# Kernel optimization log

Hardware: AMD Instinct MI355X
Metric: run time of the kernel (lower is better)

Reference implementation:

```python
import jax, jax.numpy as jnp
import numpy as np

# irrep blocks for 0e+1o+2e: dims 1, 3, 5 (total D=9)
BLOCKS = [(0, 1), (1, 4), (4, 9)]

def block_linear(x, W):
    # x: [N, C, 9], W: [3, C, C] -- e3nn Linear mixes channels within each irrep block
    outs = [jnp.einsum('ncd,cq->nqd', x[..., s:e], W[l]) for l, (s, e) in enumerate(BLOCKS)]
    return jnp.concatenate(outs, axis=-1)

def setup_inputs() -> dict:
    key = jax.random.key(0)
    ks = jax.random.split(key, 14)
    N, E, C, D, B, H, Z = 16384, 262144, 32, 9, 8, 64, 4
    inp = {
        'node_feats': jax.random.normal(ks[0], (N, C, D), jnp.float32),
        'node_attrs': jax.random.uniform(ks[1], (N, Z), jnp.float32),
        'edge_feats': jax.random.normal(ks[2], (E, B), jnp.float32),
        'edge_sh': jax.random.normal(ks[3], (E, D), jnp.float32),
        'cutoff': jax.random.uniform(ks[4], (E, 1), jnp.float32),
        # learned params
        'W_up': jax.random.normal(ks[5], (3, C, C), jnp.float32) / np.float32(np.sqrt(C)),
        'W1': jax.random.normal(ks[6], (B, H), jnp.float32) / np.float32(np.sqrt(B)),
        'W2': jax.random.normal(ks[7], (H, H), jnp.float32) / np.float32(np.sqrt(H)),
        'W3': jax.random.normal(ks[8], (H, C), jnp.float32) / np.float32(np.sqrt(H)),
        'W_lin': jax.random.normal(ks[9], (3, C, C), jnp.float32) / np.float32(np.sqrt(C)),
        'W_sc': jax.random.normal(ks[10], (Z, 3, C, C), jnp.float32) / np.float32(np.sqrt(C)),
        # fixed Clebsch-Gordan-like coupling tensor (constant structure of the TP)
        'CG': jax.random.normal(ks[11], (D, D, D), jnp.float32) / np.float32(D),
        'edge_src': jax.random.randint(ks[12], (E,), 0, N, jnp.int32),
        'edge_dst': jax.random.randint(ks[13], (E,), 0, N, jnp.int32),
    }
    return inp

def reference(node_feats, node_attrs, edge_feats, edge_sh, cutoff,
              W_up, W1, W2, W3, W_lin, W_sc, CG, edge_src, edge_dst):
    N = node_feats.shape[0]
    avg_num_neighbors = 16.0
    # linear_up: per-irrep channel mixing
    x = block_linear(node_feats, W_up)
    # radial MLP -> per-edge tensor-product weights, gated by cutoff
    h = jax.nn.silu(edge_feats @ W1)
    h = jax.nn.silu(h @ W2)
    w = (h @ W3) * cutoff  # [E, C]
    # gather source node feats, weighted equivariant tensor product per edge
    xs = x[edge_src]  # [E, C, D]
    m_ij = jnp.einsum('eci,ej,ijk,ec->eck', xs, edge_sh, CG, w)  # [E, C, D]
    # scatter-sum aggregation into destination nodes
    m_i = jax.ops.segment_sum(m_ij, edge_dst, num_segments=N)  # [N, C, D]
    # output linear + neighbor normalization
    m_i = block_linear(m_i, W_lin) / avg_num_neighbors
    # element-dependent self-connection from current message
    W_node = jnp.einsum('nz,zlcq->nlcq', node_attrs, W_sc)  # [N, 3, C, C]
    scs = jnp.concatenate(
        [jnp.einsum('ncd,ncq->nqd', m_i[..., s:e], W_node[:, l]) for l, (s, e) in enumerate(BLOCKS)],
        axis=-1)
    return (m_i, scs)
```

## Files before the change

### kernel.cpp

```cpp
#include <hip/hip_runtime.h>
#include <cstdint>

#define CC 32
#define DD 9
#define CD 288
#define BB 8
#define HH 64
#define ZZ 4
#define NB 8

typedef __attribute__((ext_vector_type(8))) short bf16x8;
typedef __attribute__((ext_vector_type(4))) float f32x4;

__device__ __forceinline__ float silu_f(float v) {
  return v / (1.0f + __expf(-v));
}

__device__ __forceinline__ int blk_of(int d) { return d == 0 ? 0 : (d < 4 ? 1 : 2); }

__device__ __forceinline__ unsigned int f2bf(float f) {
  unsigned int u = __float_as_uint(f);
  return (u + 0x7fffu + ((u >> 16) & 1u)) >> 16;
}
__device__ __forceinline__ float bf_lo(unsigned int u) { return __uint_as_float(u << 16); }
__device__ __forceinline__ float bf_hi(unsigned int u) { return __uint_as_float(u & 0xffff0000u); }

__global__ __launch_bounds__(256) void k_zero(float* __restrict__ p, int n) {
  int i = blockIdx.x * 256 + threadIdx.x;
  if (i < n) p[i] = 0.0f;
}

__global__ __launch_bounds__(256) void k_hist(const int* __restrict__ edst,
                                              int* __restrict__ deg, int E) {
  int e = blockIdx.x * 256 + threadIdx.x;
  if (e < E) atomicAdd(&deg[edst[e]], 1);
}

__global__ __launch_bounds__(1024) void k_scan(const int* __restrict__ deg,
                                               int* __restrict__ offs,
                                               int* __restrict__ cursor, int N) {
  __shared__ int part[1024];
  int t = threadIdx.x;
  int chunk = (N + 1023) >> 10;
  int base = t * chunk;
  int lim = N - base; if (lim > chunk) lim = chunk; if (lim < 0) lim = 0;
  int s = 0;
  for (int i = 0; i < lim; ++i) s += deg[base + i];
  part[t] = s;
  __syncthreads();
  for (int off = 1; off < 1024; off <<= 1) {
    int v = part[t];
    int u = (t >= off) ? part[t - off] : 0;
    __syncthreads();
    part[t] = v + u;
    __syncthreads();
  }
  int run = (t == 0) ? 0 : part[t - 1];
  for (int i = 0; i < lim; ++i) {
    offs[base + i] = run;
    cursor[base + i] = run;
    run += deg[base + i];
  }
  if (t == 1023) offs[N] = run;
}

__global__ __launch_bounds__(256) void k_scatter(const int* __restrict__ edst,
                                                 const int* __restrict__ esrc,
                                                 int* __restrict__ cursor,
                                                 int* __restrict__ eidx,
                                                 int* __restrict__ srcs, int E) {
  int e = blockIdx.x * 256 + threadIdx.x;
  if (e < E) {
    int d = edst[e];
    int pos = atomicAdd(&cursor[d], 1);
    eidx[pos] = e;
    srcs[pos] = esrc[e];
  }
}

__global__ __launch_bounds__(256) void k_eshs(const int* __restrict__ eidx,
                                              const float* __restrict__ esh,
                                              unsigned int* __restrict__ esh_p, long total) {
  long i = (long)blockIdx.x * 256 + threadIdx.x;
  if (i < total) {
    long pos = i / 5;
    int jj = (int)(i - pos * 5);
    int e = eidx[pos];
    unsigned int lo = f2bf(esh[(size_t)e * 9 + 2 * jj]);
    unsigned int hi = (jj < 4) ? f2bf(esh[(size_t)e * 9 + 2 * jj + 1]) : 0u;
    esh_p[i] = lo | (hi << 16);
  }
}

__global__ __launch_bounds__(288) void k_linear_up(
    const float* __restrict__ nf, const float* __restrict__ Wup,
    unsigned int* __restrict__ x_p, int N) {
  __shared__ float snf[NB][DD * 36];
  __shared__ float sval[NB][DD][CC];
  int t = threadIdx.x;
  int g = t >> 5, q = t & 31;
  int tc = t / 9, td = t - tc * 9;
  int l0 = blk_of(g);
  float wcol[CC];
#pragma unroll
  for (int c = 0; c < CC; ++c) wcol[c] = Wup[l0 * 1024 + c * 32 + q];
  int n0 = blockIdx.x * NB;
#pragma unroll
  for (int nb = 0; nb < NB; ++nb) {
    if (n0 + nb < N) snf[nb][td * 36 + tc] = nf[(size_t)(n0 + nb) * CD + t];
  }
  __syncthreads();
#pragma unroll
  for (int nb = 0; nb < NB; ++nb) {
    if (n0 + nb >= N) break;
    const float4* rowp = (const float4*)(snf[nb] + g * 36);
    float a0 = 0.f, a1 = 0.f;
#pragma unroll
    for (int c4 = 0; c4 < 8; ++c4) {
      float4 b = rowp[c4];
      a0 += b.x * wcol[c4 * 4 + 0] + b.y * wcol[c4 * 4 + 1];
      a1 += b.z * wcol[c4 * 4 + 2] + b.w * wcol[c4 * 4 + 3];
    }
    sval[nb][g][q] = a0 + a1;
  }
  __syncthreads();
#pragma unroll
  for (int it = 0; it < 5; ++it) {
    int idx = it * 288 + t;
    if (idx < NB * 160) {
      int nb = idx / 160, r = idx - nb * 160;
      int p = r >> 5, c = r & 31;
      if (n0 + nb < N) {
        unsigned int lo = f2bf(sval[nb][2 * p][c]);
        unsigned int hi = (p < 4) ? f2bf(sval[nb][2 * p + 1][c]) : 0u;
        x_p[(size_t)(n0 + nb) * 160 + r] = lo | (hi << 16);
      }
    }
  }
}

__global__ __launch_bounds__(64) void k_mlp_mfma(
    const float* __restrict__ ef, const float* __restrict__ cut,
    const float* __restrict__ W1, const float* __restrict__ W2,
    const float* __restrict__ W3, const int* __restrict__ eidx,
    unsigned int* __restrict__ w_p, int E) {
  __shared__ ushort hbuf[4096];
  __shared__ ushort h2buf[4096];
  __shared__ float scut[64];
  int l = threadIdx.x;
  int h = l >> 4, li = l & 15;
  bf16x8 A2[4][2];
#pragma unroll
  for (int qm = 0; qm < 4; ++qm)
#pragma unroll
    for (int kb = 0; kb < 2; ++kb)
#pragma unroll
      for (int j = 0; j < 8; ++j)
        A2[qm][kb][j] = (short)f2bf(W2[(32 * kb + 8 * h + j) * HH + 16 * qm + li]);
  bf16x8 A3[2][2];
#pragma unroll
  for (int cm = 0; cm < 2; ++cm)
#pragma unroll
    for (int kb = 0; kb < 2; ++kb)
#pragma unroll
      for (int j = 0; j < 8; ++j)
        A3[cm][kb][j] = (short)f2bf(W3[(32 * kb + 8 * h + j) * CC + 16 * cm + li]);

  int ntile = E >> 6;
  for (int tile = blockIdx.x; tile < ntile; tile += gridDim.x) {
    int pos = tile * 64 + l;
    int eo = eidx[pos];
    const float4* efp = (const float4*)(ef + (size_t)eo * BB);
    float4 efa = efp[0];
    float4 efb = efp[1];
    scut[l] = cut[eo];
    float efv[BB] = {efa.x, efa.y, efa.z, efa.w, efb.x, efb.y, efb.z, efb.w};
#pragma unroll
    for (int g = 0; g < 8; ++g) {
      float hv[8];
#pragma unroll
      for (int jj = 0; jj < 8; ++jj) {
        int q = g * 8 + jj;
        float a = 0.f;
#pragma unroll
        for (int kin = 0; kin < BB; ++kin) a += efv[kin] * W1[kin * HH + q];
        hv[jj] = silu_f(a);
      }
      unsigned int d0 = f2bf(hv[0]) | (f2bf(hv[1]) << 16);
      unsigned int d1 = f2bf(hv[2]) | (f2bf(hv[3]) << 16);
      unsigned int d2 = f2bf(hv[4]) | (f2bf(hv[5]) << 16);
      unsigned int d3 = f2bf(hv[6]) | (f2bf(hv[7]) << 16);
      int F = ((l >> 4) * 2 + (g >> 2)) * 4 + (g & 3);
      *(uint4*)&hbuf[(F * 16 + li) * 8] = make_uint4(d0, d1, d2, d3);
    }
    f32x4 acc2[4][4];
#pragma unroll
    for (int qm = 0; qm < 4; ++qm)
#pragma unroll
      for (int nb = 0; nb < 4; ++nb) acc2[qm][nb] = (f32x4){0.f, 0.f, 0.f, 0.f};
#pragma unroll
    for (int nb = 0; nb < 4; ++nb)
#pragma unroll
      for (int kb = 0; kb < 2; ++kb) {
        int F = (nb * 2 + kb) * 4 + h;
        bf16x8 Bf = *(const bf16x8*)&hbuf[(F * 16 + li) * 8];
#pragma unroll
        for (int qm = 0; qm < 4; ++qm)
          acc2[qm][nb] = __builtin_amdgcn_mfma_f32_16x16x32_bf16(
              A2[qm][kb], Bf, acc2[qm][nb], 0, 0, 0);
      }
#pragma unroll
    for (int qm = 0; qm < 4; ++qm)
#pragma unroll
      for (int nb = 0; nb < 4; ++nb) {
        float v0 = silu_f(acc2[qm][nb][0]);
        float v1 = silu_f(acc2[qm][nb][1]);
        float v2 = silu_f(acc2[qm][nb][2]);
        float v3 = silu_f(acc2[qm][nb][3]);
        unsigned int lo = f2bf(v0) | (f2bf(v1) << 16);
        unsigned int hi = f2bf(v2) | (f2bf(v3) << 16);
        int G = (nb * 2 + (qm >> 1)) * 4 + ((2 * qm + (h >> 1)) & 3);
        *(uint2*)&h2buf[(G * 16 + li) * 8 + (h & 1) * 4] = make_uint2(lo, hi);
      }
    f32x4 acc3[2][4];
#pragma unroll
    for (int cm = 0; cm < 2; ++cm)
#pragma unroll
      for (int nb = 0; nb < 4; ++nb) acc3[cm][nb] = (f32x4){0.f, 0.f, 0.f, 0.f};
#pragma unroll
    for (int nb = 0; nb < 4; ++nb)
#pragma unroll
      for (int kb = 0; kb < 2; ++kb) {
        int G = (nb * 2 + kb) * 4 + h;
        bf16x8 Bf = *(const bf16x8*)&h2buf[(G * 16 + li) * 8];
#pragma unroll
        for (int cm = 0; cm < 2; ++cm)
          acc3[cm][nb] = __builtin_amdgcn_mfma_f32_16x16x32_bf16(
              A3[cm][kb], Bf, acc3[cm][nb], 0, 0, 0);
      }
#pragma unroll
    for (int nb = 0; nb < 4; ++nb) {
      float cv = scut[16 * nb + li];
#pragma unroll
      for (int cm = 0; cm < 2; ++cm) {
        unsigned int lo = f2bf(acc3[cm][nb][0] * cv) | (f2bf(acc3[cm][nb][1] * cv) << 16);
        unsigned int hi = f2bf(acc3[cm][nb][2] * cv) | (f2bf(acc3[cm][nb][3] * cv) << 16);
        *(uint2*)&w_p[(size_t)(tile * 64 + 16 * nb + li) * 16 + 8 * cm + 2 * h] =
            make_uint2(lo, hi);
      }
    }
  }
}

__global__ __launch_bounds__(256) void k_gather(
    const unsigned int* __restrict__ x_p, const unsigned int* __restrict__ w_p,
    const unsigned int* __restrict__ esh_p, const float* __restrict__ CG,
    const int* __restrict__ offs, const int* __restrict__ srcs,
    float* __restrict__ mpre, int N) {
  int wid = (blockIdx.x * 256 + threadIdx.x) >> 6;
  if (wid >= N) return;
  int lane = threadIdx.x & 63;
  int h = lane >> 5, c = lane & 31;
  int beg = offs[wid], end = offs[wid + 1];
  float P[81];
#pragma unroll
  for (int i = 0; i < 81; ++i) P[i] = 0.f;
  for (int p0 = beg; p0 < end; p0 += 2) {
    int p = p0 + h;
    bool ok = p < end;
    int pp = ok ? p : p0;
    int s = srcs[pp];
    unsigned int wu = w_p[(size_t)pp * 16 + (c >> 1)];
    float wc = ok ? ((c & 1) ? bf_hi(wu) : bf_lo(wu)) : 0.f;
    const unsigned int* shp = esh_p + (size_t)pp * 5;
    unsigned int s0 = shp[0], s1 = shp[1], s2 = shp[2], s3 = shp[3], s4 = shp[4];
    float sh[DD];
    sh[0] = bf_lo(s0); sh[1] = bf_hi(s0);
    sh[2] = bf_lo(s1); sh[3] = bf_hi(s1);
    sh[4] = bf_lo(s2); sh[5] = bf_hi(s2);
    sh[6] = bf_lo(s3); sh[7] = bf_hi(s3);
    sh[8] = bf_lo(s4);
    const unsigned int* xp = x_p + (size_t)s * 160 + c;
    unsigned int u0 = xp[0], u1 = xp[32], u2 = xp[64], u3 = xp[96], u4 = xp[128];
    float xs[DD];
    xs[0] = bf_lo(u0); xs[1] = bf_hi(u0);
    xs[2] = bf_lo(u1); xs[3] = bf_hi(u1);
    xs[4] = bf_lo(u2); xs[5] = bf_hi(u2);
    xs[6] = bf_lo(u3); xs[7] = bf_hi(u3);
    xs[8] = bf_lo(u4);
#pragma unroll
    for (int i = 0; i < DD; ++i) {
      float t = wc * xs[i];
#pragma unroll
      for (int j = 0; j < DD; ++j) P[i * DD + j] += t * sh[j];
    }
  }
  float m[DD];
#pragma unroll
  for (int k = 0; k < DD; ++k) m[k] = 0.f;
#pragma unroll
  for (int i = 0; i < DD; ++i) {
#pragma unroll
    for (int j = 0; j < DD; ++j) {
      float p = P[i * DD + j];
#pragma unroll
      for (int k = 0; k < DD; ++k) m[k] += p * CG[i * 81 + j * DD + k];
    }
  }
#pragma unroll
  for (int k = 0; k < DD; ++k) m[k] += __shfl_xor(m[k], 32);
  if (h == 0) {
    float* mp = mpre + (size_t)wid * CD + c;
#pragma unroll
    for (int k = 0; k < DD; ++k) mp[k * 32] = m[k];
  }
}

__global__ __launch_bounds__(288, 1) void k_out(
    const float* __restrict__ attrs, const float* __restrict__ Wlin,
    const float* __restrict__ Wsc,
    float* __restrict__ out1, float* __restrict__ out2, int N) {
  __shared__ float smp[NB][CD];
  __shared__ float smt[NB][CD];
  __shared__ float sres1[NB * CD];
  __shared__ float sres2[NB * CD];
  int t = threadIdx.x;
  int g = t >> 5, q = t & 31;
  int l0 = blk_of(g);
  float wl[CC];
#pragma unroll
  for (int c = 0; c < CC; ++c) wl[c] = Wlin[l0 * 1024 + c * 32 + q];
  float ws0[CC], ws1[CC], ws2[CC], ws3[CC];
#pragma unroll
  for (int c = 0; c < CC; ++c) {
    ws0[c] = Wsc[0 * 3072 + l0 * 1024 + c * 32 + q];
    ws1[c] = Wsc[1 * 3072 + l0 * 1024 + c * 32 + q];
    ws2[c] = Wsc[2 * 3072 + l0 * 1024 + c * 32 + q];
    ws3[c] = Wsc[3 * 3072 + l0 * 1024 + c * 32 + q];
  }
  int nbat = (N + NB - 1) / NB;
  int b = blockIdx.x;
  float r[NB];
  if (b < nbat) {
#pragma unroll
    for (int nb = 0; nb < NB; ++nb) r[nb] = out2[(size_t)(b * NB + nb) * CD + t];
  }
  for (; b < nbat; b += gridDim.x) {
    int n0 = b * NB;
    __syncthreads();
#pragma unroll
    for (int nb = 0; nb < NB; ++nb) smp[nb][t] = r[nb];
    float4 av[NB];
#pragma unroll
    for (int nb = 0; nb < NB; ++nb) av[nb] = ((const float4*)attrs)[n0 + nb];
    __syncthreads();
    int b2 = b + gridDim.x;
    if (b2 < nbat) {
#pragma unroll
      for (int nb = 0; nb < NB; ++nb) r[nb] = out2[(size_t)(b2 * NB + nb) * CD + t];
    }
#pragma unroll
    for (int nb = 0; nb < NB; ++nb) {
      const float4* rowp = (const float4*)(smp[nb] + g * 32);
      float b0 = 0.f, b1 = 0.f;
#pragma unroll
      for (int c4 = 0; c4 < 8; ++c4) {
        float4 bb = rowp[c4];
        b0 += bb.x * wl[c4 * 4 + 0] + bb.y * wl[c4 * 4 + 1];
        b1 += bb.z * wl[c4 * 4 + 2] + bb.w * wl[c4 * 4 + 3];
      }
      float v = (b0 + b1) * (1.0f / 16.0f);
      smt[nb][t] = v;
      sres1[nb * CD + q * DD + g] = v;
    }
    __syncthreads();
#pragma unroll
    for (int nb = 0; nb < NB; ++nb) {
      const float4* rowp = (const float4*)(smt[nb] + g * 32);
      float z0 = 0.f, z1 = 0.f, z2 = 0.f, z3 = 0.f;
#pragma unroll
      for (int c4 = 0; c4 < 8; ++c4) {
        float4 bb = rowp[c4];
#pragma unroll
        for (int j = 0; j < 4; ++j) {
          float bv = (j == 0) ? bb.x : (j == 1) ? bb.y : (j == 2) ? bb.z : bb.w;
          int c = c4 * 4 + j;
          z0 += bv * ws0[c];
          z1 += bv * ws1[c];
          z2 += bv * ws2[c];
          z3 += bv * ws3[c];
        }
      }
      float4 a = av[nb];
      sres2[nb * CD + q * DD + g] = a.x * z0 + a.y * z1 + a.z * z2 + a.w * z3;
    }
    __syncthreads();
#pragma unroll
    for (int rr = 0; rr < (NB * 72) / 288; ++rr) {
      int s = rr * 288 + t;
      int nb = s / 72, idx = s - nb * 72;
      ((float4*)(out1 + (size_t)(n0 + nb) * CD))[idx] = ((const float4*)sres1)[s];
      ((float4*)(out2 + (size_t)(n0 + nb) * CD))[idx] = ((const float4*)sres2)[s];
    }
  }
}

extern "C" void kernel_launch(void* const* d_in, const int* in_sizes, int n_in,
                              void* d_out, int out_size, void* d_ws, size_t ws_size,
                              hipStream_t stream) {
  const float* nf    = (const float*)d_in[0];
  const float* attrs = (const float*)d_in[1];
  const float* ef    = (const float*)d_in[2];
  const float* esh   = (const float*)d_in[3];
  const float* cutv  = (const float*)d_in[4];
  const float* Wup   = (const float*)d_in[5];
  const float* W1    = (const float*)d_in[6];
  const float* W2    = (const float*)d_in[7];
  const float* W3    = (const float*)d_in[8];
  const float* Wlin  = (const float*)d_in[9];
  const float* Wsc   = (const float*)d_in[10];
  const float* CG    = (const float*)d_in[11];
  const int* esrc    = (const int*)d_in[12];
  const int* edst    = (const int*)d_in[13];
  int N = in_sizes[0] / CD;
  int E = in_sizes[12];
  float* out1 = (float*)d_out;
  float* out2 = out1 + (size_t)N * CD;

  unsigned int* x_p   = (unsigned int*)d_ws;
  unsigned int* w_p   = x_p + (size_t)N * 160;
  unsigned int* esh_p = w_p + (size_t)E * 16;
  int* deg     = (int*)(esh_p + (size_t)E * 5);
  int* offs    = deg + N;
  int* cursor  = offs + N + 1;
  int* eidx    = cursor + N;
  int* srcs    = eidx + E;

  int nblk = (N + NB - 1) / NB;
  k_zero<<<(N + 255) / 256, 256, 0, stream>>>((float*)deg, N);
  k_hist<<<(E + 255) / 256, 256, 0, stream>>>(edst, deg, E);
  k_scan<<<1, 1024, 0, stream>>>(deg, offs, cursor, N);
  k_scatter<<<(E + 255) / 256, 256, 0, stream>>>(edst, esrc, cursor, eidx, srcs, E);
  k_eshs<<<(int)(((long)E * 5 + 255) / 256), 256, 0, stream>>>(eidx, esh, esh_p, (long)E * 5);
  k_linear_up<<<nblk, 288, 0, stream>>>(nf, Wup, x_p, N);
  k_mlp_mfma<<<4096, 64, 0, stream>>>(ef, cutv, W1, W2, W3, eidx, w_p, E);
  k_gather<<<(N + 3) / 4, 256, 0, stream>>>(x_p, w_p, esh_p, CG, offs, srcs, out2, N);
  k_out<<<512, 288, 0, stream>>>(attrs, Wlin, Wsc, out1, out2, N);
}
```

Baseline: 250.3 us.

## Move gather tensor-product accumulation onto fp16 MFMA with one block per node

The per-node gather kernel now uses a 256-thread block per destination node instead of one wavefront. Edges are staged into LDS in tiles of 32, with weight times x precomputed in fp16. The outer-product accumulation over edges (xw^T times sh) and the final CG contraction run as f16 MFMA instructions instead of scalar FMAs into an 81-register accumulator. Intermediate packed storage for x, w and sh switches from bf16 to fp16 so the MFMA f16 path can be used. This trades scalar ALU work and register pressure for LDS staging, extra barriers per tile and fp16 range/precision risk, and nodes with few edges leave most of each 32-edge tile empty.

```diff
diff --git a/kernel.cpp b/kernel.cpp
--- a/kernel.cpp
+++ b/kernel.cpp
@@ -1,4 +1,5 @@
 #include <hip/hip_runtime.h>
+#include <hip/hip_fp16.h>
 #include <cstdint>
 
 #define CC 32
@@ -11,6 +12,9 @@
 
 typedef __attribute__((ext_vector_type(8))) short bf16x8;
 typedef __attribute__((ext_vector_type(4))) float f32x4;
+typedef _Float16 f16x8 __attribute__((ext_vector_type(8)));
+
+union U4F16 { uint4 u; f16x8 v; };
 
 __device__ __forceinline__ float silu_f(float v) {
   return v / (1.0f + __expf(-v));
@@ -22,8 +26,6 @@
   unsigned int u = __float_as_uint(f);
   return (u + 0x7fffu + ((u >> 16) & 1u)) >> 16;
 }
-__device__ __forceinline__ float bf_lo(unsigned int u) { return __uint_as_float(u << 16); }
-__device__ __forceinline__ float bf_hi(unsigned int u) { return __uint_as_float(u & 0xffff0000u); }
 
 __global__ __launch_bounds__(256) void k_zero(float* __restrict__ p, int n) {
   int i = blockIdx.x * 256 + threadIdx.x;
@@ -86,9 +88,10 @@
     long pos = i / 5;
     int jj = (int)(i - pos * 5);
     int e = eidx[pos];
-    unsigned int lo = f2bf(esh[(size_t)e * 9 + 2 * jj]);
-    unsigned int hi = (jj < 4) ? f2bf(esh[(size_t)e * 9 + 2 * jj + 1]) : 0u;
-    esh_p[i] = lo | (hi << 16);
+    float lo = esh[(size_t)e * 9 + 2 * jj];
+    float hi = (jj < 4) ? esh[(size_t)e * 9 + 2 * jj + 1] : 0.f;
+    __half2 h = __floats2half2_rn(lo, hi);
+    esh_p[i] = *(unsigned int*)&h;
   }
 }
 
@@ -131,9 +134,10 @@
       int nb = idx / 160, r = idx - nb * 160;
       int p = r >> 5, c = r & 31;
       if (n0 + nb < N) {
-        unsigned int lo = f2bf(sval[nb][2 * p][c]);
-        unsigned int hi = (p < 4) ? f2bf(sval[nb][2 * p + 1][c]) : 0u;
-        x_p[(size_t)(n0 + nb) * 160 + r] = lo | (hi << 16);
+        float lo = sval[nb][2 * p][c];
+        float hi = (p < 4) ? sval[nb][2 * p + 1][c] : 0.f;
+        __half2 h = __floats2half2_rn(lo, hi);
+        x_p[(size_t)(n0 + nb) * 160 + r] = *(unsigned int*)&h;
       }
     }
   }
@@ -243,10 +247,10 @@
       float cv = scut[16 * nb + li];
 #pragma unroll
       for (int cm = 0; cm < 2; ++cm) {
-        unsigned int lo = f2bf(acc3[cm][nb][0] * cv) | (f2bf(acc3[cm][nb][1] * cv) << 16);
-        unsigned int hi = f2bf(acc3[cm][nb][2] * cv) | (f2bf(acc3[cm][nb][3] * cv) << 16);
+        __half2 p0 = __floats2half2_rn(acc3[cm][nb][0] * cv, acc3[cm][nb][1] * cv);
+        __half2 p1 = __floats2half2_rn(acc3[cm][nb][2] * cv, acc3[cm][nb][3] * cv);
         *(uint2*)&w_p[(size_t)(tile * 64 + 16 * nb + li) * 16 + 8 * cm + 2 * h] =
-            make_uint2(lo, hi);
+            make_uint2(*(unsigned int*)&p0, *(unsigned int*)&p1);
       }
     }
   }
@@ -257,62 +261,149 @@
     const unsigned int* __restrict__ esh_p, const float* __restrict__ CG,
     const int* __restrict__ offs, const int* __restrict__ srcs,
     float* __restrict__ mpre, int N) {
-  int wid = (blockIdx.x * 256 + threadIdx.x) >> 6;
-  if (wid >= N) return;
-  int lane = threadIdx.x & 63;
-  int h = lane >> 5, c = lane & 31;
-  int beg = offs[wid], end = offs[wid + 1];
-  float P[81];
-#pragma unroll
-  for (int i = 0; i < 81; ++i) P[i] = 0.f;
-  for (int p0 = beg; p0 < end; p0 += 2) {
-    int p = p0 + h;
-    bool ok = p < end;
-    int pp = ok ? p : p0;
-    int s = srcs[pp];
-    unsigned int wu = w_p[(size_t)pp * 16 + (c >> 1)];
-    float wc = ok ? ((c & 1) ? bf_hi(wu) : bf_lo(wu)) : 0.f;
-    const unsigned int* shp = esh_p + (size_t)pp * 5;
-    unsigned int s0 = shp[0], s1 = shp[1], s2 = shp[2], s3 = shp[3], s4 = shp[4];
-    float sh[DD];
-    sh[0] = bf_lo(s0); sh[1] = bf_hi(s0);
-    sh[2] = bf_lo(s1); sh[3] = bf_hi(s1);
-    sh[4] = bf_lo(s2); sh[5] = bf_hi(s2);
-    sh[6] = bf_lo(s3); sh[7] = bf_hi(s3);
-    sh[8] = bf_lo(s4);
-    const unsigned int* xp = x_p + (size_t)s * 160 + c;
-    unsigned int u0 = xp[0], u1 = xp[32], u2 = xp[64], u3 = xp[96], u4 = xp[128];
-    float xs[DD];
-    xs[0] = bf_lo(u0); xs[1] = bf_hi(u0);
-    xs[2] = bf_lo(u1); xs[3] = bf_hi(u1);
-    xs[4] = bf_lo(u2); xs[5] = bf_hi(u2);
-    xs[6] = bf_lo(u3); xs[7] = bf_hi(u3);
-    xs[8] = bf_lo(u4);
-#pragma unroll
-    for (int i = 0; i < DD; ++i) {
-      float t = wc * xs[i];
-#pragma unroll
-      for (int j = 0; j < DD; ++j) P[i * DD + j] += t * sh[j];
-    }
-  }
-  float m[DD];
-#pragma unroll
-  for (int k = 0; k < DD; ++k) m[k] = 0.f;
-#pragma unroll
-  for (int i = 0; i < DD; ++i) {
-#pragma unroll
-    for (int j = 0; j < DD; ++j) {
-      float p = P[i * DD + j];
-#pragma unroll
-      for (int k = 0; k < DD; ++k) m[k] += p * CG[i * 81 + j * DD + k];
-    }
-  }
-#pragma unroll
-  for (int k = 0; k < DD; ++k) m[k] += __shfl_xor(m[k], 32);
-  if (h == 0) {
-    float* mp = mpre + (size_t)wid * CD + c;
-#pragma unroll
-    for (int k = 0; k < DD; ++k) mp[k * 32] = m[k];
+  __shared__ __align__(16) ushort xw[32 * 322];
+  __shared__ __align__(16) ushort shst[32 * 16];
+  __shared__ __align__(16) ushort pbuf[32 * 104];
+  int n = blockIdx.x;
+  if (n >= N) return;
+  int t = threadIdx.x;
+  int w = t >> 6, l = t & 63;
+  int g = t >> 5, c = t & 31;
+  int beg = offs[n], end = offs[n + 1];
+  int ntiles = (end - beg + 31) >> 5;
+
+  for (int i = t; i < 32 * 52; i += 256) ((unsigned int*)pbuf)[i] = 0u;
+
+  U4F16 Bcg[3];
+#pragma unroll
+  for (int kb = 0; kb < 3; ++kb) {
+    unsigned int du[4];
+#pragma unroll
+    for (int jp = 0; jp < 4; ++jp) {
+      unsigned int dv = 0;
+#pragma unroll
+      for (int sub = 0; sub < 2; ++sub) {
+        int j = jp * 2 + sub;
+        int ij = 32 * kb + 8 * (l >> 4) + j;
+        int kout = l & 15;
+        float v = 0.f;
+        if (ij < 81 && kout < 9) v = CG[(ij / 9) * 81 + (ij % 9) * 9 + kout];
+        __half hv = __float2half_rn(v);
+        dv |= ((unsigned int)*(ushort*)&hv) << (16 * sub);
+      }
+      du[jp] = dv;
+    }
+    Bcg[kb].u = make_uint4(du[0], du[1], du[2], du[3]);
+  }
+
+  f32x4 acc[5];
+#pragma unroll
+  for (int idx = 0; idx < 5; ++idx) acc[idx] = (f32x4){0.f, 0.f, 0.f, 0.f};
+
+  __syncthreads();
+
+  for (int tile = 0; tile < ntiles; ++tile) {
+    int tb = beg + tile * 32;
+#pragma unroll
+    for (int ee = 0; ee < 4; ++ee) {
+      int e = g + 8 * ee;
+      int pos = tb + e;
+      bool ok = pos < end;
+      int pp = ok ? pos : beg;
+      int s = srcs[pp];
+      unsigned int wu = w_p[(size_t)pp * 16 + (c >> 1)];
+      __half2 wpair = *(__half2*)&wu;
+      __half wcv = (c & 1) ? wpair.y : wpair.x;
+      if (!ok) wcv = __float2half_rn(0.0f);
+      __half2 wc2 = __half2half2(wcv);
+      const unsigned int* xp = x_p + (size_t)s * 160 + c;
+      unsigned int u0 = xp[0], u1 = xp[32], u2 = xp[64], u3 = xp[96], u4 = xp[128];
+      unsigned int* xwdw = (unsigned int*)xw;
+      int basedw = e * 161 + c * 5;
+      __half2 p0 = __hmul2(wc2, *(__half2*)&u0);
+      __half2 p1 = __hmul2(wc2, *(__half2*)&u1);
+      __half2 p2 = __hmul2(wc2, *(__half2*)&u2);
+      __half2 p3 = __hmul2(wc2, *(__half2*)&u3);
+      __half2 p4 = __hmul2(wc2, *(__half2*)&u4);
+      xwdw[basedw + 0] = *(unsigned int*)&p0;
+      xwdw[basedw + 1] = *(unsigned int*)&p1;
+      xwdw[basedw + 2] = *(unsigned int*)&p2;
+      xwdw[basedw + 3] = *(unsigned int*)&p3;
+      xwdw[basedw + 4] = *(unsigned int*)&p4;
+      if (c < 5) {
+        ((unsigned int*)shst)[e * 8 + c] = esh_p[(size_t)pp * 5 + c];
+      } else if (c < 8) {
+        ((unsigned int*)shst)[e * 8 + c] = 0u;
+      }
+    }
+    __syncthreads();
+    U4F16 Bsh;
+    {
+      unsigned int du[4];
+#pragma unroll
+      for (int jp = 0; jp < 4; ++jp) {
+        ushort a = shst[(8 * (l >> 4) + 2 * jp) * 16 + (l & 15)];
+        ushort b = shst[(8 * (l >> 4) + 2 * jp + 1) * 16 + (l & 15)];
+        du[jp] = (unsigned int)a | ((unsigned int)b << 16);
+      }
+      Bsh.u = make_uint4(du[0], du[1], du[2], du[3]);
+    }
+#pragma unroll
+    for (int idx = 0; idx < 5; ++idx) {
+      int item = w + idx * 4;
+      if (item < 18) {
+        int i = item >> 1, ch = item & 1;
+        int cc = ch * 16 + (l & 15);
+        U4F16 Af;
+        unsigned int du[4];
+#pragma unroll
+        for (int jp = 0; jp < 4; ++jp) {
+          int e0 = 8 * (l >> 4) + 2 * jp;
+          ushort a = xw[e0 * 322 + cc * 10 + i];
+          ushort b = xw[(e0 + 1) * 322 + cc * 10 + i];
+          du[jp] = (unsigned int)a | ((unsigned int)b << 16);
+        }
+        Af.u = make_uint4(du[0], du[1], du[2], du[3]);
+        acc[idx] = __builtin_amdgcn_mfma_f32_16x16x32_f16(Af.v, Bsh.v, acc[idx], 0, 0, 0);
+      }
+    }
+    __syncthreads();
+  }
+
+#pragma unroll
+  for (int idx = 0; idx < 5; ++idx) {
+    int item = w + idx * 4;
+    if (item < 18) {
+      int i = item >> 1, ch = item & 1;
+      int jj = l & 15;
+      if (jj < 9) {
+#pragma unroll
+        for (int r = 0; r < 4; ++r) {
+          int crow = ch * 16 + 4 * (l >> 4) + r;
+          __half hv = __float2half_rn(acc[idx][r]);
+          pbuf[crow * 104 + i * 9 + jj] = *(ushort*)&hv;
+        }
+      }
+    }
+  }
+  __syncthreads();
+  if (w < 2) {
+    int ch = w;
+    f32x4 macc = (f32x4){0.f, 0.f, 0.f, 0.f};
+#pragma unroll
+    for (int kb = 0; kb < 3; ++kb) {
+      int cc = ch * 16 + (l & 15);
+      U4F16 Af;
+      Af.u = *(const uint4*)&((const unsigned int*)pbuf)[cc * 52 + 16 * kb + 4 * (l >> 4)];
+      macc = __builtin_amdgcn_mfma_f32_16x16x32_f16(Af.v, Bcg[kb].v, macc, 0, 0, 0);
+    }
+    int kout = l & 15;
+    if (kout < 9) {
+#pragma unroll
+      for (int r = 0; r < 4; ++r) {
+        mpre[(size_t)n * CD + kout * 32 + ch * 16 + 4 * (l >> 4) + r] = macc[r];
+      }
+    }
   }
 }
 
@@ -444,6 +535,6 @@
   k_eshs<<<(int)(((long)E * 5 + 255) / 256), 256, 0, stream>>>(eidx, esh, esh_p, (long)E * 5);
   k_linear_up<<<nblk, 288, 0, stream>>>(nf, Wup, x_p, N);
   k_mlp_mfma<<<4096, 64, 0, stream>>>(ef, cutv, W1, W2, W3, eidx, w_p, E);
-  k_gather<<<(N + 3) / 4, 256, 0, stream>>>(x_p, w_p, esh_p, CG, offs, srcs, out2, N);
+  k_gather<<<N, 256, 0, stream>>>(x_p, w_p, esh_p, CG, offs, srcs, out2, N);
   k_out<<<512, 288, 0, stream>>>(attrs, Wlin, Wsc, out1, out2, N);
 }
```

Result: slower. 367.7 us (+46.9%).
